# Kernel tuning notes

Hardware: AMD Instinct MI355X
Metric: run time of the kernel (lower is better)

The kernel has to match this reference:

```python
import jax, jax.numpy as jnp
import numpy as np

NP_, NA_ = 100_000, 50_000
E_ = 200_000
IN, HID, OUT = 128, 128, 128
HEADS = 4
D = HID // HEADS
# (src_node_type, dst_node_type) for edge types: cites, writes, written_by
EDGE_SPECS = [(0, 0), (1, 0), (0, 1)]
N_TYPES = 2
N_LAYERS = 2


def _rand_edges(key, e, n_src, n_dst):
    k1, k2 = jax.random.split(key)
    return jnp.stack([jax.random.randint(k1, (e,), 0, n_src),
                      jax.random.randint(k2, (e,), 0, n_dst)]).astype(jnp.int64)


def setup_inputs() -> dict:
    key = jax.random.key(0)
    ks = jax.random.split(key, 24)
    s = 0.05
    inp = {
        "x_paper": jax.random.normal(ks[0], (NP_, IN), jnp.float32),
        "x_author": jax.random.normal(ks[1], (NA_, IN), jnp.float32),
        "e_cites": _rand_edges(ks[2], E_, NP_, NP_),
        "e_writes": _rand_edges(ks[3], E_, NA_, NP_),
        "e_written": _rand_edges(ks[4], E_, NP_, NA_),
        # per-node-type input projection
        "lin_W": jax.random.normal(ks[5], (N_TYPES, IN, HID), jnp.float32) * s,
        "lin_b": jnp.zeros((N_TYPES, HID), jnp.float32),
        # per-layer, per-node-type K/Q/V projections
        "k_W": jax.random.normal(ks[6], (N_LAYERS, N_TYPES, HID, HID), jnp.float32) * s,
        "k_b": jnp.zeros((N_LAYERS, N_TYPES, HID), jnp.float32),
        "q_W": jax.random.normal(ks[7], (N_LAYERS, N_TYPES, HID, HID), jnp.float32) * s,
        "q_b": jnp.zeros((N_LAYERS, N_TYPES, HID), jnp.float32),
        "v_W": jax.random.normal(ks[8], (N_LAYERS, N_TYPES, HID, HID), jnp.float32) * s,
        "v_b": jnp.zeros((N_LAYERS, N_TYPES, HID), jnp.float32),
        # per-layer, per-node-type output projection a_lin
        "a_W": jax.random.normal(ks[9], (N_LAYERS, N_TYPES, HID, OUT), jnp.float32) * s,
        "a_b": jnp.zeros((N_LAYERS, N_TYPES, OUT), jnp.float32),
        # per-layer, per-node-type skip gate logit
        "skip": jnp.ones((N_LAYERS, N_TYPES), jnp.float32),
        # per-layer, per-edge-type relation matrices and priors
        "a_rel": jax.random.normal(ks[10], (N_LAYERS, 3, HEADS, D, D), jnp.float32) * s,
        "m_rel": jax.random.normal(ks[11], (N_LAYERS, 3, HEADS, D, D), jnp.float32) * s,
        "p_rel": jnp.ones((N_LAYERS, 3, HEADS), jnp.float32),
    }
    return inp


def _seg_softmax(logits, idx, n):
    m = jax.ops.segment_max(logits, idx, num_segments=n)  # [n,H]
    e = jnp.exp(logits - m[idx])
    s = jax.ops.segment_sum(e, idx, num_segments=n)
    return e / s[idx]


def _hgt_conv(xs, edges, kW, kb, qW, qb, vW, vb, aW, ab, skip, a_rel, m_rel, p_rel):
    ks = [(x @ kW[t] + kb[t]).reshape(-1, HEADS, D) for t, x in enumerate(xs)]
    qs = [(x @ qW[t] + qb[t]).reshape(-1, HEADS, D) for t, x in enumerate(xs)]
    vs = [(x @ vW[t] + vb[t]).reshape(-1, HEADS, D) for t, x in enumerate(xs)]
    acc = [jnp.zeros((x.shape[0], HEADS, D), x.dtype) for x in xs]
    scale = 1.0 / np.sqrt(D).astype(np.float32)
    for et, (s_t, d_t) in enumerate(EDGE_SPECS):
        src, dst = edges[et][0], edges[et][1]
        # relation-specific transform on the (smaller) node set, then gather
        kt = jnp.einsum('nhd,hde->nhe', ks[s_t], a_rel[et])
        vt = jnp.einsum('nhd,hde->nhe', vs[s_t], m_rel[et])
        n_dst = xs[d_t].shape[0]
        logits = (qs[d_t][dst] * kt[src]).sum(-1) * p_rel[et] * scale  # [E,H]
        att = _seg_softmax(logits, dst, n_dst)  # edge softmax per dst node (per edge type)
        msg = vt[src] * att[:, :, None]  # [E,H,D]
        acc[d_t] = acc[d_t] + jax.ops.segment_sum(msg, dst, num_segments=n_dst)
    outs = []
    for t, x in enumerate(xs):
        o = jax.nn.gelu(acc[t].reshape(x.shape[0], HID), approximate=False) @ aW[t] + ab[t]
        g = jax.nn.sigmoid(skip[t])  # out dim == in dim -> skip gate active
        outs.append(g * o + (1.0 - g) * x)
    return outs


def reference(x_paper, x_author, e_cites, e_writes, e_written,
              lin_W, lin_b, k_W, k_b, q_W, q_b, v_W, v_b,
              a_W, a_b, skip, a_rel, m_rel, p_rel):
    edges = [e_cites, e_writes, e_written]
    xs = [x_paper @ lin_W[0] + lin_b[0], x_author @ lin_W[1] + lin_b[1]]
    for L in range(N_LAYERS):
        xs = _hgt_conv(xs, edges, k_W[L], k_b[L], q_W[L], q_b[L], v_W[L], v_b[L],
                       a_W[L], a_b[L], skip[L], a_rel[L], m_rel[L], p_rel[L])
    return jnp.concatenate(xs, axis=0)  # [NP_+NA_, OUT]
```

## Files before the change

kernel.cpp:

```cpp
#include <hip/hip_runtime.h>
#include <math.h>

#define NPn 100000
#define NAn 50000
#define NTn 150000
#define En  200000
#define SCAN_N 250000

typedef short s16x8 __attribute__((ext_vector_type(8)));
typedef float f32x4 __attribute__((ext_vector_type(4)));

__device__ __forceinline__ unsigned short f2bfbits(float f) {
  unsigned u = __builtin_bit_cast(unsigned, f);
  return (unsigned short)((u + 0x7fffu + ((u >> 16) & 1u)) >> 16);
}
__device__ __forceinline__ float bf2f(unsigned short b) {
  return __builtin_bit_cast(float, (unsigned)b << 16);
}
__device__ __forceinline__ float gelu_f(float v) {
  return 0.5f * v * (1.f + erff(v * 0.70710678118654752f));
}

__device__ __forceinline__ void ldcol(const unsigned short* __restrict__ W, int lane, int ct, s16x8* b) {
  #pragma unroll
  for (int ks = 0; ks < 4; ++ks)
    b[ks] = *reinterpret_cast<const s16x8*>(W + ((size_t)(ks * 8 + ct) * 64 + lane) * 8);
}
__device__ __forceinline__ void mfma4(const s16x8* af, const s16x8* b, f32x4& acc) {
  #pragma unroll
  for (int ks = 0; ks < 4; ++ks)
    acc = __builtin_amdgcn_mfma_f32_16x16x32_bf16(af[ks], b[ks], acc, 0, 0, 0);
}

__global__ __launch_bounds__(256) void hist3_k(const int* __restrict__ e0, const int* __restrict__ e1,
                                               const int* __restrict__ e2, int* __restrict__ deg) {
  int i = blockIdx.x * 256 + threadIdx.x;
  int et = blockIdx.y;
  if (i >= En) return;
  const int* d = et == 0 ? e0 : (et == 1 ? e1 : e2);
  int etoff = et == 0 ? 0 : (et == 1 ? 100000 : 200000);
  atomicAdd(&deg[etoff + d[En + i]], 1);
}

__global__ __launch_bounds__(256) void scan1_k(const int* __restrict__ deg, int* __restrict__ bsum) {
  int t = threadIdx.x, lane = t & 63, wv = t >> 6;
  int base = blockIdx.x * 1024 + t * 4;
  int a0 = 0, a1 = 0, a2 = 0, a3 = 0;
  if (base + 3 < SCAN_N) {
    int4 v = *reinterpret_cast<const int4*>(deg + base);
    a0 = v.x; a1 = v.y; a2 = v.z; a3 = v.w;
  } else {
    if (base + 0 < SCAN_N) a0 = deg[base + 0];
    if (base + 1 < SCAN_N) a1 = deg[base + 1];
    if (base + 2 < SCAN_N) a2 = deg[base + 2];
    if (base + 3 < SCAN_N) a3 = deg[base + 3];
  }
  int s = a0 + a1 + a2 + a3;
  #pragma unroll
  for (int d = 1; d < 64; d <<= 1) s += __shfl_xor(s, d);
  __shared__ int wt[4];
  if (lane == 0) wt[wv] = s;
  __syncthreads();
  if (t == 0) bsum[blockIdx.x] = wt[0] + wt[1] + wt[2] + wt[3];
}

__global__ __launch_bounds__(256) void scan2_k(int* __restrict__ bsum, int nb) {
  int t = threadIdx.x, lane = t & 63, wv = t >> 6;
  int v = (t < nb) ? bsum[t] : 0;
  int x = v;
  #pragma unroll
  for (int d = 1; d < 64; d <<= 1) {
    int y = __shfl_up(x, d);
    if (lane >= d) x += y;
  }
  __shared__ int wt[4];
  if (lane == 63) wt[wv] = x;
  __syncthreads();
  int off = 0;
  for (int w = 0; w < wv; ++w) off += wt[w];
  if (t < nb) bsum[t] = x + off - v;
}

__global__ __launch_bounds__(256) void scan3_k(const int* __restrict__ deg, const int* __restrict__ bpre,
                                               int* __restrict__ S) {
  int t = threadIdx.x, lane = t & 63, wv = t >> 6;
  int base = blockIdx.x * 1024 + t * 4;
  int a[4] = {0, 0, 0, 0};
  if (base + 3 < SCAN_N) {
    int4 v = *reinterpret_cast<const int4*>(deg + base);
    a[0] = v.x; a[1] = v.y; a[2] = v.z; a[3] = v.w;
  } else {
    #pragma unroll
    for (int j = 0; j < 4; ++j) if (base + j < SCAN_N) a[j] = deg[base + j];
  }
  int s = a[0] + a[1] + a[2] + a[3];
  int x = s;
  #pragma unroll
  for (int d = 1; d < 64; d <<= 1) {
    int y = __shfl_up(x, d);
    if (lane >= d) x += y;
  }
  __shared__ int wt[4];
  if (lane == 63) wt[wv] = x;
  __syncthreads();
  int off = bpre[blockIdx.x];
  for (int w = 0; w < wv; ++w) off += wt[w];
  int ex = off + x - s;
  #pragma unroll
  for (int j = 0; j < 4; ++j) {
    int idx = base + j;
    if (idx < SCAN_N) {
      S[idx] = ex;
      ex += a[j];
      if (idx == SCAN_N - 1) S[SCAN_N] = ex;
    }
  }
}

__global__ __launch_bounds__(256) void fill3_k(const int* __restrict__ e0, const int* __restrict__ e1,
                                               const int* __restrict__ e2, int* cur, int* __restrict__ col) {
  int i = blockIdx.x * 256 + threadIdx.x;
  int et = blockIdx.y;
  if (i >= En) return;
  const int* ep = et == 0 ? e0 : (et == 1 ? e1 : e2);
  int etoff = et == 0 ? 0 : (et == 1 ? 100000 : 200000);
  int p = atomicAdd(&cur[etoff + ep[En + i]], 1);
  col[p] = ep[i];
}

__global__ __launch_bounds__(256) void fuse_k(const float* __restrict__ kW, const float* __restrict__ kb,
                                              const float* __restrict__ vW, const float* __restrict__ vb,
                                              const float* __restrict__ a_rel, const float* __restrict__ m_rel,
                                              float* __restrict__ Wf, float* __restrict__ bfv) {
  int b = blockIdx.x;
  int L = b / 6, et = (b % 6) / 2, which = b & 1;
  int s_t = (et == 1) ? 1 : 0;
  const float* W = which ? vW : kW;
  const float* bb = which ? vb : kb;
  const float* R = which ? m_rel : a_rel;
  const float* Wsrc = W + (size_t)(L * 2 + s_t) * 128 * 128;
  const float* bsrc = bb + (size_t)(L * 2 + s_t) * 128;
  const float* Rsrc = R + (size_t)(L * 3 + et) * 4 * 32 * 32;
  float* Wdst = Wf + (size_t)b * 128 * 128;
  float* bdst = bfv + (size_t)b * 128;
  for (int idx = threadIdx.x; idx < 128 * 128; idx += 256) {
    int i = idx >> 7, c = idx & 127;
    int h = c >> 5, cc = c & 31;
    const float* r = Rsrc + (size_t)h * 32 * 32 + cc;
    const float* w = Wsrc + (size_t)i * 128 + h * 32;
    float s = 0.f;
    #pragma unroll 8
    for (int d = 0; d < 32; ++d) s += w[d] * r[d * 32];
    Wdst[idx] = s;
  }
  for (int c = threadIdx.x; c < 128; c += 256) {
    int h = c >> 5, cc = c & 31;
    float s = 0.f;
    for (int d = 0; d < 32; ++d) s += bsrc[h * 32 + d] * Rsrc[((size_t)h * 32 + d) * 32 + cc];
    bdst[c] = s;
  }
}

__global__ __launch_bounds__(256) void pack_k(const float* __restrict__ linW, const float* __restrict__ qW,
                                              const float* __restrict__ aW, const float* __restrict__ Wf,
                                              unsigned short* __restrict__ Wp) {
  int m = blockIdx.x;
  const float* src;
  if (m < 2) src = linW + (size_t)m * 16384;
  else if (m < 6) src = qW + (size_t)(m - 2) * 16384;
  else if (m < 18) src = Wf + (size_t)(m - 6) * 16384;
  else src = aW + (size_t)(m - 18) * 16384;
  int lane = threadIdx.x & 63, wv = threadIdx.x >> 6;
  unsigned short* dst = Wp + (size_t)m * 16384;
  for (int ct = 0; ct < 8; ++ct) {
    s16x8 t;
    #pragma unroll
    for (int i = 0; i < 8; ++i) {
      int k = wv * 32 + (lane >> 4) * 8 + i;
      int n = ct * 16 + (lane & 15);
      t[i] = (short)f2bfbits(src[k * 128 + n]);
    }
    *reinterpret_cast<s16x8*>(dst + ((size_t)(wv * 8 + ct) * 64 + lane) * 8) = t;
  }
}

struct IJob { const float* X; const unsigned short* W; const float* bias; unsigned short* Y; int N; };

__global__ __launch_bounds__(256, 4) void iproj_k(IJob ja, IJob jb) {
  IJob j = blockIdx.y ? jb : ja;
  int ntj = (j.N + 63) >> 6;
  int tile = blockIdx.x;
  if (tile >= ntj) return;
  int lane = threadIdx.x & 63, wv = threadIdx.x >> 6;
  int t = threadIdx.x;
  int rl = j.N - tile * 64; if (rl > 64) rl = 64;

  __shared__ float xin[64 * 132];
  {
    const uint4* src = reinterpret_cast<const uint4*>(j.X + (size_t)tile * 64 * 128);
    uint4* dst = reinterpret_cast<uint4*>(xin);
    for (int c = t; c < 2048; c += 256) {
      int row = c >> 5;
      if (row < rl) dst[row * 33 + (c & 31)] = src[c];
    }
  }
  __syncthreads();

  int lr = wv * 16 + (lane & 15);
  s16x8 af[4];
  #pragma unroll
  for (int ks = 0; ks < 4; ++ks) {
    const float* p = xin + lr * 132 + (lane >> 4) * 8 + ks * 32;
    s16x8 tt;
    #pragma unroll
    for (int i = 0; i < 8; ++i) tt[i] = (short)f2bfbits(p[i]);
    af[ks] = tt;
  }

  float bias_[8];
  #pragma unroll
  for (int ct = 0; ct < 8; ++ct) bias_[ct] = j.bias[ct * 16 + (lane & 15)];

  f32x4 acc[8];
  #pragma unroll
  for (int ct = 0; ct < 8; ++ct) acc[ct] = (f32x4){0.f, 0.f, 0.f, 0.f};

  s16x8 bA[4], bB[4];
  ldcol(j.W, lane, 0, bA);
  ldcol(j.W, lane, 1, bB);
  mfma4(af, bA, acc[0]); ldcol(j.W, lane, 2, bA);
  mfma4(af, bB, acc[1]); ldcol(j.W, lane, 3, bB);
  mfma4(af, bA, acc[2]); ldcol(j.W, lane, 4, bA);
  mfma4(af, bB, acc[3]); ldcol(j.W, lane, 5, bB);
  mfma4(af, bA, acc[4]); ldcol(j.W, lane, 6, bA);
  mfma4(af, bB, acc[5]); ldcol(j.W, lane, 7, bB);
  mfma4(af, bA, acc[6]);
  mfma4(af, bB, acc[7]);

  __syncthreads();
  unsigned short* ot = reinterpret_cast<unsigned short*>(xin);
  int c0 = lane & 15, r00 = wv * 16 + (lane >> 4) * 4;
  #pragma unroll
  for (int ct = 0; ct < 8; ++ct)
    #pragma unroll
    for (int i = 0; i < 4; ++i)
      ot[(r00 + i) * 132 + ct * 16 + c0] = f2bfbits(acc[ct][i] + bias_[ct]);
  __syncthreads();
  {
    unsigned int* dstU = reinterpret_cast<unsigned int*>(j.Y + (size_t)tile * 64 * 128);
    for (int c = t; c < 4096; c += 256) {
      int row = c >> 6, col2 = c & 63;
      if (row < rl) dstU[row * 64 + col2] = *reinterpret_cast<const unsigned int*>(ot + row * 132 + col2 * 2);
    }
  }
}

struct QKVJob {
  const unsigned short* X; int N; int nm; int pad;
  const unsigned short* W[5];
  const float* bias[5];
  unsigned short* Y[5];
};

__global__ __launch_bounds__(256, 4) void qkv_k(QKVJob ja, QKVJob jb) {
  QKVJob j = blockIdx.y ? jb : ja;
  int ntj = (j.N + 63) >> 6;
  int tile = blockIdx.x;
  if (tile >= ntj) return;
  int lane = threadIdx.x & 63, wv = threadIdx.x >> 6;
  int t = threadIdx.x;
  int rl = j.N - tile * 64; if (rl > 64) rl = 64;

  int arow = tile * 64 + wv * 16 + (lane & 15);
  if (arow >= j.N) arow = j.N - 1;
  const unsigned short* xp = j.X + (size_t)arow * 128 + (lane >> 4) * 8;
  s16x8 af[4];
  #pragma unroll
  for (int ks = 0; ks < 4; ++ks) af[ks] = *reinterpret_cast<const s16x8*>(xp + ks * 32);

  __shared__ unsigned short ot[64 * 132];
  int c0 = lane & 15, r00 = wv * 16 + (lane >> 4) * 4;

  s16x8 bA[4], bB[4];
  ldcol(j.W[0], lane, 0, bA);

  for (int m = 0; m < j.nm; ++m) {
    const unsigned short* Wm = j.W[m];
    float bias_[8];
    #pragma unroll
    for (int ct = 0; ct < 8; ++ct) bias_[ct] = j.bias[m][ct * 16 + (lane & 15)];

    f32x4 acc[8];
    #pragma unroll
    for (int ct = 0; ct < 8; ++ct) acc[ct] = (f32x4){0.f, 0.f, 0.f, 0.f};

    ldcol(Wm, lane, 1, bB);
    mfma4(af, bA, acc[0]); ldcol(Wm, lane, 2, bA);
    mfma4(af, bB, acc[1]); ldcol(Wm, lane, 3, bB);
    mfma4(af, bA, acc[2]); ldcol(Wm, lane, 4, bA);
    mfma4(af, bB, acc[3]); ldcol(Wm, lane, 5, bB);
    mfma4(af, bA, acc[4]); ldcol(Wm, lane, 6, bA);
    mfma4(af, bB, acc[5]); ldcol(Wm, lane, 7, bB);
    mfma4(af, bA, acc[6]);
    if (m + 1 < j.nm) ldcol(j.W[m + 1], lane, 0, bA);
    mfma4(af, bB, acc[7]);

    if (m) __syncthreads();
    #pragma unroll
    for (int ct = 0; ct < 8; ++ct)
      #pragma unroll
      for (int i = 0; i < 4; ++i)
        ot[(r00 + i) * 132 + ct * 16 + c0] = f2bfbits(acc[ct][i] + bias_[ct]);
    __syncthreads();
    unsigned int* dstU = reinterpret_cast<unsigned int*>(j.Y[m] + (size_t)tile * 64 * 128);
    for (int c = t; c < 4096; c += 256) {
      int row = c >> 6, col2 = c & 63;
      if (row < rl) dstU[row * 64 + col2] = *reinterpret_cast<const unsigned int*>(ot + row * 132 + col2 * 2);
    }
  }
}

struct OJob {
  const unsigned short* G;
  const unsigned short* W;
  const float* bias;
  const unsigned short* skip;
  const float* skp;
  unsigned short* Yb;
  float* Yf;
  int N;
};

template <int FINAL>
__global__ __launch_bounds__(256, 4) void oproj_k(OJob ja, OJob jb) {
  OJob j = blockIdx.y ? jb : ja;
  int ntj = (j.N + 63) >> 6;
  int tile = blockIdx.x;
  if (tile >= ntj) return;
  int lane = threadIdx.x & 63, wv = threadIdx.x >> 6;
  int t = threadIdx.x;
  int rl = j.N - tile * 64; if (rl > 64) rl = 64;

  __shared__ unsigned short sk[64 * 132];
  {
    const unsigned int* srcU = reinterpret_cast<const unsigned int*>(j.skip + (size_t)tile * 64 * 128);
    for (int c = t; c < 4096; c += 256) {
      int row = c >> 6, col2 = c & 63;
      if (row < rl) *reinterpret_cast<unsigned int*>(sk + row * 132 + col2 * 2) = srcU[row * 64 + col2];
    }
  }

  int arow = tile * 64 + wv * 16 + (lane & 15);
  if (arow >= j.N) arow = j.N - 1;
  const unsigned short* xp = j.G + (size_t)arow * 128 + (lane >> 4) * 8;
  s16x8 af[4];
  #pragma unroll
  for (int ks = 0; ks < 4; ++ks) af[ks] = *reinterpret_cast<const s16x8*>(xp + ks * 32);

  float bias_[8];
  #pragma unroll
  for (int ct = 0; ct < 8; ++ct) bias_[ct] = j.bias[ct * 16 + (lane & 15)];
  float g = 1.f / (1.f + __expf(-*j.skp));

  f32x4 acc[8];
  #pragma unroll
  for (int ct = 0; ct < 8; ++ct) acc[ct] = (f32x4){0.f, 0.f, 0.f, 0.f};

  s16x8 bA[4], bB[4];
  ldcol(j.W, lane, 0, bA);
  ldcol(j.W, lane, 1, bB);
  mfma4(af, bA, acc[0]); ldcol(j.W, lane, 2, bA);
  mfma4(af, bB, acc[1]); ldcol(j.W, lane, 3, bB);
  mfma4(af, bA, acc[2]); ldcol(j.W, lane, 4, bA);
  mfma4(af, bB, acc[3]); ldcol(j.W, lane, 5, bB);
  mfma4(af, bA, acc[4]); ldcol(j.W, lane, 6, bA);
  mfma4(af, bB, acc[5]); ldcol(j.W, lane, 7, bB);
  mfma4(af, bA, acc[6]);
  mfma4(af, bB, acc[7]);

  __syncthreads();
  int c0 = lane & 15, r00 = wv * 16 + (lane >> 4) * 4;
  if (FINAL) {
    float* yf = j.Yf + (size_t)tile * 64 * 128;
    #pragma unroll
    for (int ct = 0; ct < 8; ++ct)
      #pragma unroll
      for (int i = 0; i < 4; ++i) {
        int r = r00 + i;
        if (r < rl) {
          float y = g * (acc[ct][i] + bias_[ct]) + (1.f - g) * bf2f(sk[r * 132 + ct * 16 + c0]);
          yf[r * 128 + ct * 16 + c0] = y;
        }
      }
  } else {
    #pragma unroll
    for (int ct = 0; ct < 8; ++ct)
      #pragma unroll
      for (int i = 0; i < 4; ++i) {
        int idx = (r00 + i) * 132 + ct * 16 + c0;
        float y = g * (acc[ct][i] + bias_[ct]) + (1.f - g) * bf2f(sk[idx]);
        sk[idx] = f2bfbits(y);
      }
    __syncthreads();
    unsigned int* dstU = reinterpret_cast<unsigned int*>(j.Yb + (size_t)tile * 64 * 128);
    for (int c = t; c < 4096; c += 256) {
      int row = c >> 6, col2 = c & 63;
      if (row < rl) dstU[row * 64 + col2] = *reinterpret_cast<const unsigned int*>(sk + row * 132 + col2 * 2);
    }
  }
}

template <int NPARTS>
__global__ __launch_bounds__(256) void attn_k(const int* __restrict__ S, const int* __restrict__ col,
                                              const unsigned short* __restrict__ kt,
                                              const unsigned short* __restrict__ vt,
                                              const unsigned short* __restrict__ qb,
                                              unsigned short* __restrict__ gbuf,
                                              const float* __restrict__ prp0, const float* __restrict__ prp1,
                                              int n_dst, int qbase, int soff0, int soff1,
                                              int ktbase0, int ktbase1) {
  int node = (blockIdx.x * 256 + threadIdx.x) >> 6;
  if (node >= n_dst) return;
  int lane = threadIdx.x & 63;
  int h = lane >> 4;

  ushort2 qv = *reinterpret_cast<const ushort2*>(qb + (size_t)(qbase + node) * 128 + lane * 2);
  float q0 = bf2f(qv.x), q1 = bf2f(qv.y);

  float facc0 = 0.f, facc1 = 0.f;
  #pragma unroll
  for (int p = 0; p < NPARTS; ++p) {
    int soff = p ? soff1 : soff0;
    const unsigned short* ktb = kt + (size_t)(p ? ktbase1 : ktbase0) * 128;
    const unsigned short* vtb = vt + (size_t)(p ? ktbase1 : ktbase0) * 128;
    const float* prp = p ? prp1 : prp0;
    float pr = prp[h] * 0.17677669529663687f;
    int rs = S[soff + node], re = S[soff + node + 1];
    if (rs < re) {
      float m = -3.0e38f, den = 0.f, n0 = 0.f, n1 = 0.f;
      for (int i = rs; i < re; ++i) {
        int s = col[i];
        ushort2 kv = *reinterpret_cast<const ushort2*>(ktb + (size_t)s * 128 + lane * 2);
        float pdot = q0 * bf2f(kv.x) + q1 * bf2f(kv.y);
        pdot += __shfl_xor(pdot, 1); pdot += __shfl_xor(pdot, 2);
        pdot += __shfl_xor(pdot, 4); pdot += __shfl_xor(pdot, 8);
        float pm = pdot * pr;
        ushort2 vv = *reinterpret_cast<const ushort2*>(vtb + (size_t)s * 128 + lane * 2);
        float nm = fmaxf(m, pm);
        float sc = __expf(m - nm);
        float w = __expf(pm - nm);
        den = den * sc + w;
        n0 = n0 * sc + w * bf2f(vv.x);
        n1 = n1 * sc + w * bf2f(vv.y);
        m = nm;
      }
      float inv = 1.f / den;
      facc0 += n0 * inv;
      facc1 += n1 * inv;
    }
  }
  ushort2 o;
  o.x = f2bfbits(gelu_f(facc0));
  o.y = f2bfbits(gelu_f(facc1));
  *reinterpret_cast<ushort2*>(gbuf + (size_t)(qbase + node) * 128 + lane * 2) = o;
}

extern "C" void kernel_launch(void* const* d_in, const int* in_sizes, int n_in,
                              void* d_out, int out_size, void* d_ws, size_t ws_size,
                              hipStream_t stream) {
  const float* x_paper  = (const float*)d_in[0];
  const float* x_author = (const float*)d_in[1];
  const int* e[3] = {(const int*)d_in[2], (const int*)d_in[3], (const int*)d_in[4]};
  const float* linW = (const float*)d_in[5];
  const float* linb = (const float*)d_in[6];
  const float* kW = (const float*)d_in[7];
  const float* kb = (const float*)d_in[8];
  const float* qW = (const float*)d_in[9];
  const float* qbv = (const float*)d_in[10];
  const float* vW = (const float*)d_in[11];
  const float* vb = (const float*)d_in[12];
  const float* aW = (const float*)d_in[13];
  const float* ab = (const float*)d_in[14];
  const float* skipv = (const float*)d_in[15];
  const float* a_rel = (const float*)d_in[16];
  const float* m_rel = (const float*)d_in[17];
  const float* prel  = (const float*)d_in[18];

  char* ws = (char*)d_ws;
  size_t off = 0;
  auto alloc = [&](size_t b) { char* p = ws + off; off = (off + b + 255) & ~(size_t)255; return p; };
  unsigned short* qbuf = (unsigned short*)alloc((size_t)NTn * 128 * 2);
  unsigned short* ktA  = (unsigned short*)alloc((size_t)SCAN_N * 128 * 2);
  unsigned short* vtA  = (unsigned short*)alloc((size_t)SCAN_N * 128 * 2);
  unsigned short* gbuf = (unsigned short*)alloc((size_t)NTn * 128 * 2);
  unsigned short* xb   = (unsigned short*)alloc((size_t)NTn * 128 * 2);
  int* deg   = (int*)alloc((size_t)SCAN_N * 4);
  int* cur   = (int*)alloc((size_t)SCAN_N * 4);
  int* S     = (int*)alloc((size_t)(SCAN_N + 1) * 4);
  int* bsum  = (int*)alloc(256 * 4);
  int* col   = (int*)alloc((size_t)3 * En * 4);
  float* Wf  = (float*)alloc((size_t)12 * 16384 * 4);
  float* bfv = (float*)alloc((size_t)12 * 128 * 4);
  unsigned short* Wp = (unsigned short*)alloc((size_t)22 * 16384 * 2);

  hipMemsetAsync(deg, 0, (size_t)SCAN_N * 4, stream);
  hist3_k<<<dim3(782, 3), 256, 0, stream>>>(e[0], e[1], e[2], deg);
  scan1_k<<<245, 256, 0, stream>>>(deg, bsum);
  scan2_k<<<1, 256, 0, stream>>>(bsum, 245);
  scan3_k<<<245, 256, 0, stream>>>(deg, bsum, S);
  hipMemcpyAsync(cur, S, (size_t)SCAN_N * 4, hipMemcpyDeviceToDevice, stream);
  fill3_k<<<dim3(782, 3), 256, 0, stream>>>(e[0], e[1], e[2], cur, col);

  fuse_k<<<12, 256, 0, stream>>>(kW, kb, vW, vb, a_rel, m_rel, Wf, bfv);
  pack_k<<<22, 256, 0, stream>>>(linW, qW, aW, Wf, Wp);

  const dim3 gg(1563, 2);

  {
    IJob jp  = {x_paper,  Wp + 0 * 16384, linb,        xb,                       NPn};
    IJob jat = {x_author, Wp + 1 * 16384, linb + 128,  xb + (size_t)NPn * 128,   NAn};
    iproj_k<<<gg, 256, 0, stream>>>(jp, jat);
  }

  const int ktbases[3] = {0, 100000, 150000};

  for (int L = 0; L < 2; ++L) {
    {
      QKVJob jp{}, jat{};
      jp.X = xb; jp.N = NPn; jp.nm = 5;
      jp.W[0] = Wp + (size_t)(2 + L * 2) * 16384;      jp.bias[0] = qbv + (L * 2) * 128;             jp.Y[0] = qbuf;
      jp.W[1] = Wp + (size_t)(6 + L * 6 + 0) * 16384;  jp.bias[1] = bfv + (size_t)(L * 6 + 0) * 128; jp.Y[1] = ktA + (size_t)ktbases[0] * 128;
      jp.W[2] = Wp + (size_t)(6 + L * 6 + 1) * 16384;  jp.bias[2] = bfv + (size_t)(L * 6 + 1) * 128; jp.Y[2] = vtA + (size_t)ktbases[0] * 128;
      jp.W[3] = Wp + (size_t)(6 + L * 6 + 4) * 16384;  jp.bias[3] = bfv + (size_t)(L * 6 + 4) * 128; jp.Y[3] = ktA + (size_t)ktbases[2] * 128;
      jp.W[4] = Wp + (size_t)(6 + L * 6 + 5) * 16384;  jp.bias[4] = bfv + (size_t)(L * 6 + 5) * 128; jp.Y[4] = vtA + (size_t)ktbases[2] * 128;
      jat.X = xb + (size_t)NPn * 128; jat.N = NAn; jat.nm = 3;
      jat.W[0] = Wp + (size_t)(3 + L * 2) * 16384;     jat.bias[0] = qbv + (L * 2 + 1) * 128;         jat.Y[0] = qbuf + (size_t)NPn * 128;
      jat.W[1] = Wp + (size_t)(6 + L * 6 + 2) * 16384; jat.bias[1] = bfv + (size_t)(L * 6 + 2) * 128; jat.Y[1] = ktA + (size_t)ktbases[1] * 128;
      jat.W[2] = Wp + (size_t)(6 + L * 6 + 3) * 16384; jat.bias[2] = bfv + (size_t)(L * 6 + 3) * 128; jat.Y[2] = vtA + (size_t)ktbases[1] * 128;
      qkv_k<<<gg, 256, 0, stream>>>(jp, jat);
    }
    attn_k<2><<<25000, 256, 0, stream>>>(S, col, ktA, vtA, qbuf, gbuf,
                                         prel + (size_t)(L * 3 + 0) * 4, prel + (size_t)(L * 3 + 1) * 4,
                                         NPn, 0, 0, 100000, ktbases[0], ktbases[1]);
    attn_k<1><<<12500, 256, 0, stream>>>(S, col, ktA, vtA, qbuf, gbuf,
                                         prel + (size_t)(L * 3 + 2) * 4, nullptr,
                                         NAn, NPn, 200000, 0, ktbases[2], 0);
    {
      OJob jp  = {gbuf, Wp + (size_t)(18 + L * 2) * 16384, ab + (L * 2) * 128,
                  xb, skipv + L * 2, xb, (float*)d_out, NPn};
      OJob jat = {gbuf + (size_t)NPn * 128, Wp + (size_t)(19 + L * 2) * 16384, ab + (L * 2 + 1) * 128,
                  xb + (size_t)NPn * 128, skipv + L * 2 + 1, xb + (size_t)NPn * 128,
                  (float*)d_out + (size_t)NPn * 128, NAn};
      if (L == 0) oproj_k<0><<<gg, 256, 0, stream>>>(jp, jat);
      else        oproj_k<1><<<gg, 256, 0, stream>>>(jp, jat);
    }
  }
}
```

Before: 725.8 us.

## Double QKV row tile, merge attention launches, batch edge gathers

The QKV projection now handles 128 rows per block, two 64-row halves that share each loaded weight column, so weight fragment loads are amortised over twice as many MFMAs. This costs more registers and LDS, and launch bounds drop from 4 to 3 blocks per SM. The two per-node-type attention launches become one launch over all 150k destination nodes, with the edge-type parameters chosen at runtime. The edge loop now gathers column indices and K/V values four edges at a time to increase memory-level parallelism in the irregular gathers.

```diff
diff --git a/kernel.cpp b/kernel.cpp
--- a/kernel.cpp
+++ b/kernel.cpp
@@ -262,23 +262,31 @@
   unsigned short* Y[5];
 };
 
-__global__ __launch_bounds__(256, 4) void qkv_k(QKVJob ja, QKVJob jb) {
+__global__ __launch_bounds__(256, 3) void qkv_k(QKVJob ja, QKVJob jb) {
   QKVJob j = blockIdx.y ? jb : ja;
-  int ntj = (j.N + 63) >> 6;
+  int ntj = (j.N + 127) >> 7;
   int tile = blockIdx.x;
   if (tile >= ntj) return;
   int lane = threadIdx.x & 63, wv = threadIdx.x >> 6;
   int t = threadIdx.x;
-  int rl = j.N - tile * 64; if (rl > 64) rl = 64;
-
-  int arow = tile * 64 + wv * 16 + (lane & 15);
-  if (arow >= j.N) arow = j.N - 1;
-  const unsigned short* xp = j.X + (size_t)arow * 128 + (lane >> 4) * 8;
-  s16x8 af[4];
-  #pragma unroll
-  for (int ks = 0; ks < 4; ++ks) af[ks] = *reinterpret_cast<const s16x8*>(xp + ks * 32);
-
-  __shared__ unsigned short ot[64 * 132];
+  int rbase = tile * 128;
+  int rl = j.N - rbase; if (rl > 128) rl = 128;
+
+  s16x8 af0[4], af1[4];
+  {
+    int ar = rbase + wv * 16 + (lane & 15); if (ar >= j.N) ar = j.N - 1;
+    const unsigned short* xp = j.X + (size_t)ar * 128 + (lane >> 4) * 8;
+    #pragma unroll
+    for (int ks = 0; ks < 4; ++ks) af0[ks] = *reinterpret_cast<const s16x8*>(xp + ks * 32);
+  }
+  {
+    int ar = rbase + 64 + wv * 16 + (lane & 15); if (ar >= j.N) ar = j.N - 1;
+    const unsigned short* xp = j.X + (size_t)ar * 128 + (lane >> 4) * 8;
+    #pragma unroll
+    for (int ks = 0; ks < 4; ++ks) af1[ks] = *reinterpret_cast<const s16x8*>(xp + ks * 32);
+  }
+
+  __shared__ unsigned short ot[2][64 * 132];
   int c0 = lane & 15, r00 = wv * 16 + (lane >> 4) * 4;
 
   s16x8 bA[4], bB[4];
@@ -290,32 +298,36 @@
     #pragma unroll
     for (int ct = 0; ct < 8; ++ct) bias_[ct] = j.bias[m][ct * 16 + (lane & 15)];
 
-    f32x4 acc[8];
-    #pragma unroll
-    for (int ct = 0; ct < 8; ++ct) acc[ct] = (f32x4){0.f, 0.f, 0.f, 0.f};
+    f32x4 acc0[8], acc1[8];
+    #pragma unroll
+    for (int ct = 0; ct < 8; ++ct) { acc0[ct] = (f32x4){0.f, 0.f, 0.f, 0.f}; acc1[ct] = (f32x4){0.f, 0.f, 0.f, 0.f}; }
 
     ldcol(Wm, lane, 1, bB);
-    mfma4(af, bA, acc[0]); ldcol(Wm, lane, 2, bA);
-    mfma4(af, bB, acc[1]); ldcol(Wm, lane, 3, bB);
-    mfma4(af, bA, acc[2]); ldcol(Wm, lane, 4, bA);
-    mfma4(af, bB, acc[3]); ldcol(Wm, lane, 5, bB);
-    mfma4(af, bA, acc[4]); ldcol(Wm, lane, 6, bA);
-    mfma4(af, bB, acc[5]); ldcol(Wm, lane, 7, bB);
-    mfma4(af, bA, acc[6]);
+    mfma4(af0, bA, acc0[0]); mfma4(af1, bA, acc1[0]); ldcol(Wm, lane, 2, bA);
+    mfma4(af0, bB, acc0[1]); mfma4(af1, bB, acc1[1]); ldcol(Wm, lane, 3, bB);
+    mfma4(af0, bA, acc0[2]); mfma4(af1, bA, acc1[2]); ldcol(Wm, lane, 4, bA);
+    mfma4(af0, bB, acc0[3]); mfma4(af1, bB, acc1[3]); ldcol(Wm, lane, 5, bB);
+    mfma4(af0, bA, acc0[4]); mfma4(af1, bA, acc1[4]); ldcol(Wm, lane, 6, bA);
+    mfma4(af0, bB, acc0[5]); mfma4(af1, bB, acc1[5]); ldcol(Wm, lane, 7, bB);
+    mfma4(af0, bA, acc0[6]); mfma4(af1, bA, acc1[6]);
     if (m + 1 < j.nm) ldcol(j.W[m + 1], lane, 0, bA);
-    mfma4(af, bB, acc[7]);
+    mfma4(af0, bB, acc0[7]); mfma4(af1, bB, acc1[7]);
 
     if (m) __syncthreads();
     #pragma unroll
     for (int ct = 0; ct < 8; ++ct)
       #pragma unroll
-      for (int i = 0; i < 4; ++i)
-        ot[(r00 + i) * 132 + ct * 16 + c0] = f2bfbits(acc[ct][i] + bias_[ct]);
+      for (int i = 0; i < 4; ++i) {
+        ot[0][(r00 + i) * 132 + ct * 16 + c0] = f2bfbits(acc0[ct][i] + bias_[ct]);
+        ot[1][(r00 + i) * 132 + ct * 16 + c0] = f2bfbits(acc1[ct][i] + bias_[ct]);
+      }
     __syncthreads();
-    unsigned int* dstU = reinterpret_cast<unsigned int*>(j.Y[m] + (size_t)tile * 64 * 128);
-    for (int c = t; c < 4096; c += 256) {
+    unsigned int* dstU = reinterpret_cast<unsigned int*>(j.Y[m] + (size_t)rbase * 128);
+    for (int c = t; c < 8192; c += 256) {
       int row = c >> 6, col2 = c & 63;
-      if (row < rl) dstU[row * 64 + col2] = *reinterpret_cast<const unsigned int*>(ot + row * 132 + col2 * 2);
+      if (row < rl)
+        dstU[row * 64 + col2] =
+            *reinterpret_cast<const unsigned int*>(&ot[row >> 6][(row & 63) * 132 + col2 * 2]);
     }
   }
 }
@@ -410,59 +422,70 @@
   }
 }
 
-template <int NPARTS>
 __global__ __launch_bounds__(256) void attn_k(const int* __restrict__ S, const int* __restrict__ col,
                                               const unsigned short* __restrict__ kt,
                                               const unsigned short* __restrict__ vt,
                                               const unsigned short* __restrict__ qb,
                                               unsigned short* __restrict__ gbuf,
-                                              const float* __restrict__ prp0, const float* __restrict__ prp1,
-                                              int n_dst, int qbase, int soff0, int soff1,
-                                              int ktbase0, int ktbase1) {
+                                              const float* __restrict__ prelL) {
   int node = (blockIdx.x * 256 + threadIdx.x) >> 6;
-  if (node >= n_dst) return;
+  if (node >= NTn) return;
   int lane = threadIdx.x & 63;
   int h = lane >> 4;
-
-  ushort2 qv = *reinterpret_cast<const ushort2*>(qb + (size_t)(qbase + node) * 128 + lane * 2);
+  bool isP = node < NPn;
+  int ln = isP ? node : node - NPn;
+
+  ushort2 qv = *reinterpret_cast<const ushort2*>(qb + (size_t)node * 128 + lane * 2);
   float q0 = bf2f(qv.x), q1 = bf2f(qv.y);
 
   float facc0 = 0.f, facc1 = 0.f;
-  #pragma unroll
-  for (int p = 0; p < NPARTS; ++p) {
-    int soff = p ? soff1 : soff0;
-    const unsigned short* ktb = kt + (size_t)(p ? ktbase1 : ktbase0) * 128;
-    const unsigned short* vtb = vt + (size_t)(p ? ktbase1 : ktbase0) * 128;
-    const float* prp = p ? prp1 : prp0;
+  int np = isP ? 2 : 1;
+  for (int p = 0; p < np; ++p) {
+    int soff   = isP ? (p ? 100000 : 0) : 200000;
+    int ktbase = isP ? (p ? 100000 : 0) : 150000;
+    const float* prp = prelL + (isP ? p * 4 : 8);
     float pr = prp[h] * 0.17677669529663687f;
-    int rs = S[soff + node], re = S[soff + node + 1];
-    if (rs < re) {
-      float m = -3.0e38f, den = 0.f, n0 = 0.f, n1 = 0.f;
-      for (int i = rs; i < re; ++i) {
-        int s = col[i];
-        ushort2 kv = *reinterpret_cast<const ushort2*>(ktb + (size_t)s * 128 + lane * 2);
-        float pdot = q0 * bf2f(kv.x) + q1 * bf2f(kv.y);
-        pdot += __shfl_xor(pdot, 1); pdot += __shfl_xor(pdot, 2);
-        pdot += __shfl_xor(pdot, 4); pdot += __shfl_xor(pdot, 8);
-        float pm = pdot * pr;
-        ushort2 vv = *reinterpret_cast<const ushort2*>(vtb + (size_t)s * 128 + lane * 2);
-        float nm = fmaxf(m, pm);
-        float sc = __expf(m - nm);
-        float w = __expf(pm - nm);
-        den = den * sc + w;
-        n0 = n0 * sc + w * bf2f(vv.x);
-        n1 = n1 * sc + w * bf2f(vv.y);
-        m = nm;
+    int rs = S[soff + ln], re = S[soff + ln + 1];
+    if (rs >= re) continue;
+    const unsigned short* ktb = kt + (size_t)ktbase * 128;
+    const unsigned short* vtb = vt + (size_t)ktbase * 128;
+    float m = -3.0e38f, den = 0.f, n0 = 0.f, n1 = 0.f;
+    for (int base = rs; base < re; base += 4) {
+      int n = re - base; if (n > 4) n = 4;
+      int sidx[4];
+      #pragma unroll
+      for (int jj = 0; jj < 4; ++jj) sidx[jj] = col[base + (jj < n ? jj : 0)];
+      ushort2 kvv[4], vvv[4];
+      #pragma unroll
+      for (int jj = 0; jj < 4; ++jj) {
+        kvv[jj] = *reinterpret_cast<const ushort2*>(ktb + (size_t)sidx[jj] * 128 + lane * 2);
+        vvv[jj] = *reinterpret_cast<const ushort2*>(vtb + (size_t)sidx[jj] * 128 + lane * 2);
       }
-      float inv = 1.f / den;
-      facc0 += n0 * inv;
-      facc1 += n1 * inv;
-    }
+      #pragma unroll
+      for (int jj = 0; jj < 4; ++jj) {
+        if (jj < n) {
+          float pdot = q0 * bf2f(kvv[jj].x) + q1 * bf2f(kvv[jj].y);
+          pdot += __shfl_xor(pdot, 1); pdot += __shfl_xor(pdot, 2);
+          pdot += __shfl_xor(pdot, 4); pdot += __shfl_xor(pdot, 8);
+          float pm = pdot * pr;
+          float nm = fmaxf(m, pm);
+          float sc = __expf(m - nm);
+          float w = __expf(pm - nm);
+          den = den * sc + w;
+          n0 = n0 * sc + w * bf2f(vvv[jj].x);
+          n1 = n1 * sc + w * bf2f(vvv[jj].y);
+          m = nm;
+        }
+      }
+    }
+    float inv = 1.f / den;
+    facc0 += n0 * inv;
+    facc1 += n1 * inv;
   }
   ushort2 o;
   o.x = f2bfbits(gelu_f(facc0));
   o.y = f2bfbits(gelu_f(facc1));
-  *reinterpret_cast<ushort2*>(gbuf + (size_t)(qbase + node) * 128 + lane * 2) = o;
+  *reinterpret_cast<ushort2*>(gbuf + (size_t)node * 128 + lane * 2) = o;
 }
 
 extern "C" void kernel_launch(void* const* d_in, const int* in_sizes, int n_in,
@@ -514,12 +537,10 @@
   fuse_k<<<12, 256, 0, stream>>>(kW, kb, vW, vb, a_rel, m_rel, Wf, bfv);
   pack_k<<<22, 256, 0, stream>>>(linW, qW, aW, Wf, Wp);
 
-  const dim3 gg(1563, 2);
-
   {
     IJob jp  = {x_paper,  Wp + 0 * 16384, linb,        xb,                       NPn};
     IJob jat = {x_author, Wp + 1 * 16384, linb + 128,  xb + (size_t)NPn * 128,   NAn};
-    iproj_k<<<gg, 256, 0, stream>>>(jp, jat);
+    iproj_k<<<dim3(1563, 2), 256, 0, stream>>>(jp, jat);
   }
 
   const int ktbases[3] = {0, 100000, 150000};
@@ -537,22 +558,17 @@
       jat.W[0] = Wp + (size_t)(3 + L * 2) * 16384;     jat.bias[0] = qbv + (L * 2 + 1) * 128;         jat.Y[0] = qbuf + (size_t)NPn * 128;
       jat.W[1] = Wp + (size_t)(6 + L * 6 + 2) * 16384; jat.bias[1] = bfv + (size_t)(L * 6 + 2) * 128; jat.Y[1] = ktA + (size_t)ktbases[1] * 128;
       jat.W[2] = Wp + (size_t)(6 + L * 6 + 3) * 16384; jat.bias[2] = bfv + (size_t)(L * 6 + 3) * 128; jat.Y[2] = vtA + (size_t)ktbases[1] * 128;
-      qkv_k<<<gg, 256, 0, stream>>>(jp, jat);
-    }
-    attn_k<2><<<25000, 256, 0, stream>>>(S, col, ktA, vtA, qbuf, gbuf,
-                                         prel + (size_t)(L * 3 + 0) * 4, prel + (size_t)(L * 3 + 1) * 4,
-                                         NPn, 0, 0, 100000, ktbases[0], ktbases[1]);
-    attn_k<1><<<12500, 256, 0, stream>>>(S, col, ktA, vtA, qbuf, gbuf,
-                                         prel + (size_t)(L * 3 + 2) * 4, nullptr,
-                                         NAn, NPn, 200000, 0, ktbases[2], 0);
+      qkv_k<<<dim3(782, 2), 256, 0, stream>>>(jp, jat);
+    }
+    attn_k<<<37500, 256, 0, stream>>>(S, col, ktA, vtA, qbuf, gbuf, prel + (size_t)L * 12);
     {
       OJob jp  = {gbuf, Wp + (size_t)(18 + L * 2) * 16384, ab + (L * 2) * 128,
                   xb, skipv + L * 2, xb, (float*)d_out, NPn};
       OJob jat = {gbuf + (size_t)NPn * 128, Wp + (size_t)(19 + L * 2) * 16384, ab + (L * 2 + 1) * 128,
                   xb + (size_t)NPn * 128, skipv + L * 2 + 1, xb + (size_t)NPn * 128,
                   (float*)d_out + (size_t)NPn * 128, NAn};
-      if (L == 0) oproj_k<0><<<gg, 256, 0, stream>>>(jp, jat);
-      else        oproj_k<1><<<gg, 256, 0, stream>>>(jp, jat);
-    }
-  }
-}
+      if (L == 0) oproj_k<0><<<dim3(1563, 2), 256, 0, stream>>>(jp, jat);
+      else        oproj_k<1><<<dim3(1563, 2), 256, 0, stream>>>(jp, jat);
+    }
+  }
+}
```

Result: faster. 673.2 us (-7.2%).
